# Performance work log

Measured on AMD Instinct MI355X. Metric: run time of the kernel, lower is better.

The kernel has to match this reference:

```python
import jax, jax.numpy as jnp
import numpy as np

MAX_STEPS = 20  # matches init kwarg max_steps


def gru_cell(x, h, W_ih, W_hh, b_ih, b_hh):
    # PyTorch GRUCell: gates ordered (reset, update, new)
    H = h.shape[1]
    gx = x @ W_ih.T + b_ih          # [B, 3H]
    gh = h @ W_hh.T + b_hh          # [B, 3H]
    r = jax.nn.sigmoid(gx[:, :H] + gh[:, :H])
    z = jax.nn.sigmoid(gx[:, H:2 * H] + gh[:, H:2 * H])
    n = jnp.tanh(gx[:, 2 * H:] + r * gh[:, 2 * H:])
    return (1.0 - z) * n + z * h


def setup_inputs() -> dict:
    key = jax.random.key(0)
    ks = jax.random.split(key, 10)
    B, E, H = 2048, 512, 1024
    bound = 1.0 / np.sqrt(H)  # torch default init scale
    uni = lambda k, shape: jax.random.uniform(k, shape, jnp.float32, -bound, bound)
    return {
        "x": jax.random.normal(ks[0], (B, E), jnp.float32),
        "W_ih": uni(ks[1], (3 * H, E)),
        "W_hh": uni(ks[2], (3 * H, H)),
        "b_ih": uni(ks[3], (3 * H,)),
        "b_hh": uni(ks[4], (3 * H,)),
        "w_out": uni(ks[5], (H,)),
        "b_out": uni(ks[6], (1,)),
        "w_lam": uni(ks[7], (H,)),
        "b_lam": uni(ks[8], (1,)),
        "u": jax.random.uniform(ks[9], (MAX_STEPS, B), jnp.float32),  # bernoulli draws
    }


def reference(x, W_ih, W_hh, b_ih, b_hh, w_out, b_out, w_lam, b_lam, u):
    B = x.shape[0]
    dt = x.dtype
    H = W_hh.shape[1]
    h0 = gru_cell(x, jnp.zeros((B, H), dt), W_ih, W_hh, b_ih, b_hh)
    steps = jnp.arange(1, MAX_STEPS + 1)

    def step(carry, inp):
        h, un_halted, halted, p_m, y_m = carry
        n_idx, u_n = inp
        lam_sig = jax.nn.sigmoid(h @ w_lam + b_lam[0])           # [B]
        lam = jnp.where(n_idx == MAX_STEPS, jnp.ones_like(lam_sig), lam_sig)
        y_n = h @ w_out + b_out[0]                                # [B]
        p_n = un_halted * lam
        un_halted = un_halted * (1.0 - lam)
        halt = (u_n < lam).astype(dt) * (1.0 - halted)            # bernoulli(lam)
        p_m = p_m * (1.0 - halt) + p_n * halt
        y_m = y_m * (1.0 - halt) + y_n * halt
        halted = halted + halt
        h = gru_cell(x, h, W_ih, W_hh, b_ih, b_hh)
        return (h, un_halted, halted, p_m, y_m), (p_n, y_n)

    init = (h0,
            jnp.ones((B,), dt),
            jnp.zeros((B,), dt),
            jnp.zeros((B,), dt),
            jnp.zeros((B,), dt))
    (_, _, _, p_m, y_m), (p, y) = jax.lax.scan(step, init, (steps, u))
    return p, y, p_m, y_m
```

## Files before the change

### kernel.cpp

```cpp
#include <hip/hip_runtime.h>
#include <math.h>


#define B_N 2048
#define E_N 512
#define H_N 1024
#define G3  3072
#define NSTEPS 20
#define BK 32
#define NT (H_N / BK)

typedef __attribute__((ext_vector_type(8))) _Float16 f16x8;
typedef __attribute__((ext_vector_type(4))) _Float16 f16x4v;
typedef __attribute__((ext_vector_type(4))) float    f32x4;

#define GLDS(src, dst) \
  __builtin_amdgcn_global_load_lds( \
      (const __attribute__((address_space(1))) void*)(src), \
      (__attribute__((address_space(3))) void*)(dst), 16, 0, 0)

__device__ __forceinline__ float sigmoidf_(float x) { return 1.0f / (1.0f + expf(-x)); }

__global__ __launch_bounds__(256, 1)
void gemm_step_mfma(const _Float16* __restrict__ h_hi_in,
                    const _Float16* __restrict__ h_lo_in,
                    const _Float16* __restrict__ Whi,
                    const _Float16* __restrict__ Wlo,
                    const float* __restrict__ b_hh,
                    const float* __restrict__ gx,
                    _Float16* __restrict__ h_hi_out,
                    _Float16* __restrict__ h_lo_out)
{
  __shared__ _Float16 lds[2][20480];

  const int tid  = threadIdx.x;
  const int lane = tid & 63;
  const int wv   = tid >> 6;
  const int wr   = wv >> 1;
  const int wc   = wv & 1;
  const int row0 = blockIdx.y * 128;
  const int col0 = blockIdx.x * 64;

  const _Float16* srcp[10];
  int ldsoff[10];
  #pragma unroll
  for (int j = 0; j < 10; ++j) {
    const int c   = wv * 10 + j;
    const int seg = (lane & 3) * 8;
    const _Float16* s;
    if (c < 8) {
      const int row = c * 16 + (lane >> 2);
      s = h_hi_in + (size_t)(row0 + row) * H_N + seg;
    } else if (c < 16) {
      const int row = (c - 8) * 16 + (lane >> 2);
      s = h_lo_in + (size_t)(row0 + row) * H_N + seg;
    } else if (c < 28) {
      const int br   = (c - 16) * 16 + (lane >> 2);
      const int wrow = (br >> 6) * H_N + col0 + (br & 63);
      s = Whi + (size_t)wrow * H_N + seg;
    } else {
      const int br   = (c - 28) * 16 + (lane >> 2);
      const int wrow = (br >> 6) * H_N + col0 + (br & 63);
      s = Wlo + (size_t)wrow * H_N + seg;
    }
    srcp[j]   = s;
    ldsoff[j] = c * 512;
  }

  f32x4 acc[3][4][2];
  #pragma unroll
  for (int g = 0; g < 3; ++g)
    #pragma unroll
    for (int mi = 0; mi < 4; ++mi)
      #pragma unroll
      for (int ni = 0; ni < 2; ++ni)
        acc[g][mi][ni] = (f32x4){0.f, 0.f, 0.f, 0.f};

  const int lrow = lane & 15;
  const int lk   = (lane >> 4) * 8;

  #pragma unroll
  for (int j = 0; j < 10; ++j) {
    GLDS(srcp[j], &lds[0][ldsoff[j]]);
    srcp[j] += BK;
  }
  __syncthreads();

  for (int t = 0; t < NT; ++t) {
    const int p = t & 1;
    if (t + 1 < NT) {
      #pragma unroll
      for (int j = 0; j < 10; ++j) {
        GLDS(srcp[j], &lds[p ^ 1][ldsoff[j]]);
        srcp[j] += BK;
      }
    }
    f16x8 ah[4], al[4];
    #pragma unroll
    for (int mi = 0; mi < 4; ++mi) {
      const int r = wr * 64 + mi * 16 + lrow;
      ah[mi] = *(const f16x8*)&lds[p][r * 32 + lk];
      al[mi] = *(const f16x8*)&lds[p][4096 + r * 32 + lk];
    }
    f16x8 bh[3][2], bl[3][2];
    #pragma unroll
    for (int g = 0; g < 3; ++g)
      #pragma unroll
      for (int ni = 0; ni < 2; ++ni) {
        const int r = g * 64 + wc * 32 + ni * 16 + lrow;
        bh[g][ni] = *(const f16x8*)&lds[p][8192 + r * 32 + lk];
        bl[g][ni] = *(const f16x8*)&lds[p][14336 + r * 32 + lk];
      }
    #pragma unroll
    for (int g = 0; g < 3; ++g)
      #pragma unroll
      for (int mi = 0; mi < 4; ++mi)
        #pragma unroll
        for (int ni = 0; ni < 2; ++ni) {
          f32x4 c = acc[g][mi][ni];
          c = __builtin_amdgcn_mfma_f32_16x16x32_f16(ah[mi], bh[g][ni], c, 0, 0, 0);
          c = __builtin_amdgcn_mfma_f32_16x16x32_f16(ah[mi], bl[g][ni], c, 0, 0, 0);
          c = __builtin_amdgcn_mfma_f32_16x16x32_f16(al[mi], bh[g][ni], c, 0, 0, 0);
          acc[g][mi][ni] = c;
        }
    __syncthreads();
  }

  #pragma unroll
  for (int mi = 0; mi < 4; ++mi) {
    #pragma unroll
    for (int ni = 0; ni < 2; ++ni) {
      const int n = col0 + wc * 32 + ni * 16 + lrow;
      const float bhr = b_hh[n];
      const float bhz = b_hh[H_N + n];
      const float bhn = b_hh[2 * H_N + n];
      #pragma unroll
      for (int r = 0; r < 4; ++r) {
        const int m = row0 + wr * 64 + mi * 16 + (lane >> 4) * 4 + r;
        const float gr = acc[0][mi][ni][r] + bhr;
        const float gz = acc[1][mi][ni][r] + bhz;
        const float gn = acc[2][mi][ni][r] + bhn;
        const size_t gxb = (size_t)m * G3;
        const float rr = sigmoidf_(gx[gxb + n] + gr);
        const float zz = sigmoidf_(gx[gxb + H_N + n] + gz);
        const float nn = tanhf(gx[gxb + 2 * H_N + n] + rr * gn);
        const size_t hidx = (size_t)m * H_N + n;
        const float hold = (float)h_hi_in[hidx] + (float)h_lo_in[hidx];
        const float hf = (1.f - zz) * nn + zz * hold;
        const _Float16 hh = (_Float16)hf;
        h_hi_out[hidx] = hh;
        h_lo_out[hidx] = (_Float16)(hf - (float)hh);
      }
    }
  }
}

__global__ __launch_bounds__(256)
void split_whh_kernel(const float* __restrict__ W_hh,
                      _Float16* __restrict__ Whi, _Float16* __restrict__ Wlo)
{
  const size_t base = ((size_t)blockIdx.x * 256 + threadIdx.x) * 4;
  const float4 w = *(const float4*)&W_hh[base];
  float s[4] = {w.x, w.y, w.z, w.w};
  f16x4v hi, lo;
  #pragma unroll
  for (int e = 0; e < 4; ++e) {
    const _Float16 h = (_Float16)s[e];
    hi[e] = h;
    lo[e] = (_Float16)(s[e] - (float)h);
  }
  *(f16x4v*)&Whi[base] = hi;
  *(f16x4v*)&Wlo[base] = lo;
}

__global__ __launch_bounds__(256)
void gemm_gx_kernel(const float* __restrict__ x,
                    const float* __restrict__ W_ih,
                    const float* __restrict__ b_ih,
                    float* __restrict__ gx)
{
    __shared__ float As[16][68];
    __shared__ float Bs[16][68];
    const int tid = threadIdx.x;
    const int tx = tid & 15, ty = tid >> 4;
    const int row0 = blockIdx.y * 64;
    const int col0 = blockIdx.x * 64;
    const int lr = tid >> 2;
    const int lk = (tid & 3) << 2;
    float acc[4][4] = {};
    for (int k0 = 0; k0 < E_N; k0 += 16) {
        float4 av = *(const float4*)(x    + (size_t)(row0 + lr) * E_N + k0 + lk);
        float4 bv = *(const float4*)(W_ih + (size_t)(col0 + lr) * E_N + k0 + lk);
        As[lk+0][lr] = av.x; As[lk+1][lr] = av.y; As[lk+2][lr] = av.z; As[lk+3][lr] = av.w;
        Bs[lk+0][lr] = bv.x; Bs[lk+1][lr] = bv.y; Bs[lk+2][lr] = bv.z; Bs[lk+3][lr] = bv.w;
        __syncthreads();
        #pragma unroll
        for (int k = 0; k < 16; ++k) {
            float4 a4 = *(const float4*)&As[k][ty << 2];
            float4 b4 = *(const float4*)&Bs[k][tx << 2];
            float aa[4] = {a4.x, a4.y, a4.z, a4.w};
            float bb[4] = {b4.x, b4.y, b4.z, b4.w};
            #pragma unroll
            for (int i = 0; i < 4; ++i)
                #pragma unroll
                for (int j = 0; j < 4; ++j)
                    acc[i][j] = fmaf(aa[i], bb[j], acc[i][j]);
        }
        __syncthreads();
    }
    #pragma unroll
    for (int i = 0; i < 4; ++i) {
        const int r = row0 + (ty << 2) + i;
        #pragma unroll
        for (int j = 0; j < 4; ++j) {
            const int c = col0 + (tx << 2) + j;
            gx[(size_t)r * G3 + c] = acc[i][j] + b_ih[c];
        }
    }
}

__global__ __launch_bounds__(256)
void init_h0_kernel(const float* __restrict__ gx, const float* __restrict__ b_hh,
                    _Float16* __restrict__ h_hi, _Float16* __restrict__ h_lo,
                    float* __restrict__ states)
{
    const int idx = blockIdx.x * 256 + threadIdx.x;
    const int r = idx >> 10;
    const int c = idx & (H_N - 1);
    const float rr = sigmoidf_(gx[(size_t)r * G3 + c] + b_hh[c]);
    const float zz = sigmoidf_(gx[(size_t)r * G3 + H_N + c] + b_hh[H_N + c]);
    const float nn = tanhf(gx[(size_t)r * G3 + 2 * H_N + c] + rr * b_hh[2 * H_N + c]);
    const float hf = (1.0f - zz) * nn;
    const _Float16 hh = (_Float16)hf;
    h_hi[idx] = hh;
    h_lo[idx] = (_Float16)(hf - (float)hh);
    if (idx < B_N) {
        states[idx]           = 1.0f;
        states[B_N + idx]     = 0.0f;
        states[2 * B_N + idx] = 0.0f;
        states[3 * B_N + idx] = 0.0f;
    }
}

__global__ __launch_bounds__(256)
void halt_kernel(const int n,
                 const _Float16* __restrict__ h_hi, const _Float16* __restrict__ h_lo,
                 const float* __restrict__ w_out, const float* __restrict__ b_out,
                 const float* __restrict__ w_lam, const float* __restrict__ b_lam,
                 const float* __restrict__ u,
                 float* __restrict__ states,
                 float* __restrict__ out_p, float* __restrict__ out_y,
                 float* __restrict__ out_pm, float* __restrict__ out_ym)
{
    const int row = blockIdx.x;
    const int tid = threadIdx.x;
    const size_t base = (size_t)row * H_N + (tid << 2);
    const f16x4v hh4 = *(const f16x4v*)&h_hi[base];
    const f16x4v hl4 = *(const f16x4v*)&h_lo[base];
    const float4 wl = *(const float4*)&w_lam[tid << 2];
    const float4 wo = *(const float4*)&w_out[tid << 2];
    float hv[4];
    #pragma unroll
    for (int e = 0; e < 4; ++e) hv[e] = (float)hh4[e] + (float)hl4[e];
    float s_lam = hv[0] * wl.x + hv[1] * wl.y + hv[2] * wl.z + hv[3] * wl.w;
    float s_out = hv[0] * wo.x + hv[1] * wo.y + hv[2] * wo.z + hv[3] * wo.w;
    #pragma unroll
    for (int off = 32; off > 0; off >>= 1) {
        s_lam += __shfl_down(s_lam, off);
        s_out += __shfl_down(s_out, off);
    }
    __shared__ float redl[4], redo[4];
    const int wid = tid >> 6;
    if ((tid & 63) == 0) { redl[wid] = s_lam; redo[wid] = s_out; }
    __syncthreads();
    if (tid == 0) {
        const float dlam = redl[0] + redl[1] + redl[2] + redl[3];
        const float dout = redo[0] + redo[1] + redo[2] + redo[3];
        const float lam = (n == NSTEPS) ? 1.0f : sigmoidf_(dlam + b_lam[0]);
        const float y_n = dout + b_out[0];
        float un = states[row];
        float ha = states[B_N + row];
        float pm = states[2 * B_N + row];
        float ym = states[3 * B_N + row];
        const float p_n = un * lam;
        un = un * (1.0f - lam);
        const float halt = (u[(size_t)(n - 1) * B_N + row] < lam ? 1.0f : 0.0f) * (1.0f - ha);
        pm = pm * (1.0f - halt) + p_n * halt;
        ym = ym * (1.0f - halt) + y_n * halt;
        ha += halt;
        states[row] = un;
        states[B_N + row] = ha;
        states[2 * B_N + row] = pm;
        states[3 * B_N + row] = ym;
        out_p[(size_t)(n - 1) * B_N + row] = p_n;
        out_y[(size_t)(n - 1) * B_N + row] = y_n;
        if (n == NSTEPS) { out_pm[row] = pm; out_ym[row] = ym; }
    }
}

extern "C" void kernel_launch(void* const* d_in, const int* in_sizes, int n_in,
                              void* d_out, int out_size, void* d_ws, size_t ws_size,
                              hipStream_t stream) {
    const float* x     = (const float*)d_in[0];
    const float* W_ih  = (const float*)d_in[1];
    const float* W_hh  = (const float*)d_in[2];
    const float* b_ih  = (const float*)d_in[3];
    const float* b_hh  = (const float*)d_in[4];
    const float* w_out = (const float*)d_in[5];
    const float* b_out = (const float*)d_in[6];
    const float* w_lam = (const float*)d_in[7];
    const float* b_lam = (const float*)d_in[8];
    const float* u     = (const float*)d_in[9];

    float* out_p  = (float*)d_out;
    float* out_y  = out_p + (size_t)NSTEPS * B_N;
    float* out_pm = out_y + (size_t)NSTEPS * B_N;
    float* out_ym = out_pm + B_N;

    float* ws = (float*)d_ws;
    float*     gx   = ws;
    _Float16*  Whi  = (_Float16*)(gx + (size_t)B_N * G3);
    _Float16*  Wlo  = Whi + (size_t)G3 * H_N;
    _Float16*  hAhi = Wlo + (size_t)G3 * H_N;
    _Float16*  hAlo = hAhi + (size_t)B_N * H_N;
    _Float16*  hBhi = hAlo + (size_t)B_N * H_N;
    _Float16*  hBlo = hBhi + (size_t)B_N * H_N;
    float*     states = (float*)(hBlo + (size_t)B_N * H_N);

    const dim3 blk(256);
    split_whh_kernel<<<dim3((size_t)G3 * H_N / 1024), blk, 0, stream>>>(W_hh, Whi, Wlo);
    gemm_gx_kernel<<<dim3(G3 / 64, B_N / 64), blk, 0, stream>>>(x, W_ih, b_ih, gx);
    init_h0_kernel<<<dim3(B_N * H_N / 256), blk, 0, stream>>>(gx, b_hh, hAhi, hAlo, states);

    _Float16 *hchi = hAhi, *hclo = hAlo, *hnhi = hBhi, *hnlo = hBlo;
    for (int n = 1; n <= NSTEPS; ++n) {
        halt_kernel<<<dim3(B_N), blk, 0, stream>>>(n, hchi, hclo, w_out, b_out, w_lam, b_lam, u,
                                                   states, out_p, out_y, out_pm, out_ym);
        if (n < NSTEPS) {
            gemm_step_mfma<<<dim3(H_N / 64, B_N / 128), blk, 0, stream>>>(
                hchi, hclo, Whi, Wlo, b_hh, gx, hnhi, hnlo);
            _Float16* t;
            t = hchi; hchi = hnhi; hnhi = t;
            t = hclo; hclo = hnlo; hnlo = t;
        }
    }
}
```

Before: 1.282 ms.

## Fuse halting dot products into GRU step GEMM, narrow tiles, MFMA input GEMM

Result: no change. 1.286 ms (+0.3%).

```diff
diff --git a/kernel.cpp b/kernel.cpp
--- a/kernel.cpp
+++ b/kernel.cpp
@@ -8,7 +8,9 @@
 #define G3  3072
 #define NSTEPS 20
 #define BK 32
-#define NT (H_N / BK)
+#define NT_H (H_N / BK)
+#define NT_E (E_N / BK)
+#define NCB  (H_N / 32)
 
 typedef __attribute__((ext_vector_type(8))) _Float16 f16x8;
 typedef __attribute__((ext_vector_type(4))) _Float16 f16x4v;
@@ -21,17 +23,157 @@
 
 __device__ __forceinline__ float sigmoidf_(float x) { return 1.0f / (1.0f + expf(-x)); }
 
-__global__ __launch_bounds__(256, 1)
+__global__ __launch_bounds__(256, 2)
 void gemm_step_mfma(const _Float16* __restrict__ h_hi_in,
                     const _Float16* __restrict__ h_lo_in,
                     const _Float16* __restrict__ Whi,
                     const _Float16* __restrict__ Wlo,
                     const float* __restrict__ b_hh,
                     const float* __restrict__ gx,
+                    const float* __restrict__ w_lam,
+                    const float* __restrict__ w_out,
                     _Float16* __restrict__ h_hi_out,
-                    _Float16* __restrict__ h_lo_out)
-{
-  __shared__ _Float16 lds[2][20480];
+                    _Float16* __restrict__ h_lo_out,
+                    float* __restrict__ part_lam,
+                    float* __restrict__ part_out)
+{
+  __shared__ _Float16 lds[2][14336];
+  __shared__ float pl_red[128][2], po_red[128][2];
+
+  const int tid  = threadIdx.x;
+  const int lane = tid & 63;
+  const int wv   = tid >> 6;
+  const int wr   = wv >> 1;
+  const int wc   = wv & 1;
+  const int row0 = blockIdx.y * 128;
+  const int col0 = blockIdx.x * 32;
+  const int cb   = blockIdx.x;
+
+  const _Float16* srcp[7];
+  int ldsoff[7];
+  #pragma unroll
+  for (int j = 0; j < 7; ++j) {
+    const int c     = wv * 7 + j;
+    const int seg   = (lane & 3) * 8;
+    const int row16 = lane >> 2;
+    const _Float16* s;
+    if (c < 8) {
+      s = h_hi_in + (size_t)(row0 + c * 16 + row16) * H_N + seg;
+    } else if (c < 16) {
+      s = h_lo_in + (size_t)(row0 + (c - 8) * 16 + row16) * H_N + seg;
+    } else if (c < 22) {
+      const int br = (c - 16) * 16 + row16;
+      s = Whi + (size_t)((br >> 5) * H_N + col0 + (br & 31)) * H_N + seg;
+    } else {
+      const int br = (c - 22) * 16 + row16;
+      s = Wlo + (size_t)((br >> 5) * H_N + col0 + (br & 31)) * H_N + seg;
+    }
+    srcp[j]   = s;
+    ldsoff[j] = c * 512;
+  }
+
+  f32x4 acc[3][4];
+  #pragma unroll
+  for (int g = 0; g < 3; ++g)
+    #pragma unroll
+    for (int mi = 0; mi < 4; ++mi)
+      acc[g][mi] = (f32x4){0.f, 0.f, 0.f, 0.f};
+
+  const int lrow = lane & 15;
+  const int lk   = (lane >> 4) * 8;
+  const int q    = lane >> 4;
+
+  #pragma unroll
+  for (int j = 0; j < 7; ++j) { GLDS(srcp[j], &lds[0][ldsoff[j]]); srcp[j] += BK; }
+  __syncthreads();
+
+  for (int t = 0; t < NT_H; ++t) {
+    const int p = t & 1;
+    if (t + 1 < NT_H) {
+      #pragma unroll
+      for (int j = 0; j < 7; ++j) { GLDS(srcp[j], &lds[p ^ 1][ldsoff[j]]); srcp[j] += BK; }
+    }
+    f16x8 ah[4], al[4];
+    #pragma unroll
+    for (int mi = 0; mi < 4; ++mi) {
+      const int r = wr * 64 + mi * 16 + lrow;
+      ah[mi] = *(const f16x8*)&lds[p][r * 32 + lk];
+      al[mi] = *(const f16x8*)&lds[p][4096 + r * 32 + lk];
+    }
+    f16x8 bh[3], bl[3];
+    #pragma unroll
+    for (int g = 0; g < 3; ++g) {
+      const int r = g * 32 + wc * 16 + lrow;
+      bh[g] = *(const f16x8*)&lds[p][8192 + r * 32 + lk];
+      bl[g] = *(const f16x8*)&lds[p][11264 + r * 32 + lk];
+    }
+    #pragma unroll
+    for (int g = 0; g < 3; ++g)
+      #pragma unroll
+      for (int mi = 0; mi < 4; ++mi) {
+        f32x4 c = acc[g][mi];
+        c = __builtin_amdgcn_mfma_f32_16x16x32_f16(ah[mi], bh[g], c, 0, 0, 0);
+        c = __builtin_amdgcn_mfma_f32_16x16x32_f16(ah[mi], bl[g], c, 0, 0, 0);
+        c = __builtin_amdgcn_mfma_f32_16x16x32_f16(al[mi], bh[g], c, 0, 0, 0);
+        acc[g][mi] = c;
+      }
+    __syncthreads();
+  }
+
+  const int n   = col0 + wc * 16 + lrow;
+  const float bhr = b_hh[n];
+  const float bhz = b_hh[H_N + n];
+  const float bhn = b_hh[2 * H_N + n];
+  const float wl  = w_lam[n];
+  const float wo  = w_out[n];
+  #pragma unroll
+  for (int mi = 0; mi < 4; ++mi) {
+    #pragma unroll
+    for (int r = 0; r < 4; ++r) {
+      const int m = row0 + wr * 64 + mi * 16 + q * 4 + r;
+      const float gr = acc[0][mi][r] + bhr;
+      const float gz = acc[1][mi][r] + bhz;
+      const float gn = acc[2][mi][r] + bhn;
+      const size_t gxb = (size_t)m * G3;
+      const float rr = sigmoidf_(gx[gxb + n] + gr);
+      const float zz = sigmoidf_(gx[gxb + H_N + n] + gz);
+      const float nn = tanhf(gx[gxb + 2 * H_N + n] + rr * gn);
+      const size_t hidx = (size_t)m * H_N + n;
+      const float hold = (float)h_hi_in[hidx] + (float)h_lo_in[hidx];
+      const float hf = (1.f - zz) * nn + zz * hold;
+      const _Float16 hh = (_Float16)hf;
+      h_hi_out[hidx] = hh;
+      h_lo_out[hidx] = (_Float16)(hf - (float)hh);
+      float pl = hf * wl;
+      float po = hf * wo;
+      #pragma unroll
+      for (int mk = 1; mk < 16; mk <<= 1) {
+        pl += __shfl_xor(pl, mk);
+        po += __shfl_xor(po, mk);
+      }
+      if (lrow == 0) {
+        pl_red[wr * 64 + mi * 16 + q * 4 + r][wc] = pl;
+        po_red[wr * 64 + mi * 16 + q * 4 + r][wc] = po;
+      }
+    }
+  }
+  __syncthreads();
+  if (tid < 128) {
+    const int m = row0 + tid;
+    part_lam[(size_t)cb * B_N + m] = pl_red[tid][0] + pl_red[tid][1];
+    part_out[(size_t)cb * B_N + m] = po_red[tid][0] + po_red[tid][1];
+  }
+}
+
+__global__ __launch_bounds__(256, 3)
+void gemm_gx_mfma(const _Float16* __restrict__ xhi,
+                  const _Float16* __restrict__ xlo,
+                  const _Float16* __restrict__ Wihhi,
+                  const _Float16* __restrict__ Wihlo,
+                  const float* __restrict__ b_ih,
+                  float* __restrict__ gx)
+{
+  __shared__ _Float16 lds[2][12288];
 
   const int tid  = threadIdx.x;
   const int lane = tid & 63;
@@ -41,59 +183,41 @@
   const int row0 = blockIdx.y * 128;
   const int col0 = blockIdx.x * 64;
 
-  const _Float16* srcp[10];
-  int ldsoff[10];
-  #pragma unroll
-  for (int j = 0; j < 10; ++j) {
-    const int c   = wv * 10 + j;
-    const int seg = (lane & 3) * 8;
+  const _Float16* srcp[6];
+  int ldsoff[6];
+  #pragma unroll
+  for (int j = 0; j < 6; ++j) {
+    const int c     = wv * 6 + j;
+    const int seg   = (lane & 3) * 8;
+    const int row16 = lane >> 2;
     const _Float16* s;
-    if (c < 8) {
-      const int row = c * 16 + (lane >> 2);
-      s = h_hi_in + (size_t)(row0 + row) * H_N + seg;
-    } else if (c < 16) {
-      const int row = (c - 8) * 16 + (lane >> 2);
-      s = h_lo_in + (size_t)(row0 + row) * H_N + seg;
-    } else if (c < 28) {
-      const int br   = (c - 16) * 16 + (lane >> 2);
-      const int wrow = (br >> 6) * H_N + col0 + (br & 63);
-      s = Whi + (size_t)wrow * H_N + seg;
-    } else {
-      const int br   = (c - 28) * 16 + (lane >> 2);
-      const int wrow = (br >> 6) * H_N + col0 + (br & 63);
-      s = Wlo + (size_t)wrow * H_N + seg;
-    }
+    if (c < 8)       s = xhi   + (size_t)(row0 + c * 16 + row16) * E_N + seg;
+    else if (c < 16) s = xlo   + (size_t)(row0 + (c - 8) * 16 + row16) * E_N + seg;
+    else if (c < 20) s = Wihhi + (size_t)(col0 + (c - 16) * 16 + row16) * E_N + seg;
+    else             s = Wihlo + (size_t)(col0 + (c - 20) * 16 + row16) * E_N + seg;
     srcp[j]   = s;
     ldsoff[j] = c * 512;
   }
 
-  f32x4 acc[3][4][2];
-  #pragma unroll
-  for (int g = 0; g < 3; ++g)
-    #pragma unroll
-    for (int mi = 0; mi < 4; ++mi)
-      #pragma unroll
-      for (int ni = 0; ni < 2; ++ni)
-        acc[g][mi][ni] = (f32x4){0.f, 0.f, 0.f, 0.f};
+  f32x4 acc[4][2];
+  #pragma unroll
+  for (int mi = 0; mi < 4; ++mi)
+    #pragma unroll
+    for (int ni = 0; ni < 2; ++ni) acc[mi][ni] = (f32x4){0.f, 0.f, 0.f, 0.f};
 
   const int lrow = lane & 15;
   const int lk   = (lane >> 4) * 8;
-
-  #pragma unroll
-  for (int j = 0; j < 10; ++j) {
-    GLDS(srcp[j], &lds[0][ldsoff[j]]);
-    srcp[j] += BK;
-  }
+  const int q    = lane >> 4;
+
+  #pragma unroll
+  for (int j = 0; j < 6; ++j) { GLDS(srcp[j], &lds[0][ldsoff[j]]); srcp[j] += BK; }
   __syncthreads();
 
-  for (int t = 0; t < NT; ++t) {
+  for (int t = 0; t < NT_E; ++t) {
     const int p = t & 1;
-    if (t + 1 < NT) {
-      #pragma unroll
-      for (int j = 0; j < 10; ++j) {
-        GLDS(srcp[j], &lds[p ^ 1][ldsoff[j]]);
-        srcp[j] += BK;
-      }
+    if (t + 1 < NT_E) {
+      #pragma unroll
+      for (int j = 0; j < 6; ++j) { GLDS(srcp[j], &lds[p ^ 1][ldsoff[j]]); srcp[j] += BK; }
     }
     f16x8 ah[4], al[4];
     #pragma unroll
@@ -102,27 +226,23 @@
       ah[mi] = *(const f16x8*)&lds[p][r * 32 + lk];
       al[mi] = *(const f16x8*)&lds[p][4096 + r * 32 + lk];
     }
-    f16x8 bh[3][2], bl[3][2];
-    #pragma unroll
-    for (int g = 0; g < 3; ++g)
+    f16x8 bh[2], bl[2];
+    #pragma unroll
+    for (int ni = 0; ni < 2; ++ni) {
+      const int r = wc * 32 + ni * 16 + lrow;
+      bh[ni] = *(const f16x8*)&lds[p][8192 + r * 32 + lk];
+      bl[ni] = *(const f16x8*)&lds[p][10240 + r * 32 + lk];
+    }
+    #pragma unroll
+    for (int mi = 0; mi < 4; ++mi)
       #pragma unroll
       for (int ni = 0; ni < 2; ++ni) {
-        const int r = g * 64 + wc * 32 + ni * 16 + lrow;
-        bh[g][ni] = *(const f16x8*)&lds[p][8192 + r * 32 + lk];
-        bl[g][ni] = *(const f16x8*)&lds[p][14336 + r * 32 + lk];
+        f32x4 c = acc[mi][ni];
+        c = __builtin_amdgcn_mfma_f32_16x16x32_f16(ah[mi], bh[ni], c, 0, 0, 0);
+        c = __builtin_amdgcn_mfma_f32_16x16x32_f16(ah[mi], bl[ni], c, 0, 0, 0);
+        c = __builtin_amdgcn_mfma_f32_16x16x32_f16(al[mi], bh[ni], c, 0, 0, 0);
+        acc[mi][ni] = c;
       }
-    #pragma unroll
-    for (int g = 0; g < 3; ++g)
-      #pragma unroll
-      for (int mi = 0; mi < 4; ++mi)
-        #pragma unroll
-        for (int ni = 0; ni < 2; ++ni) {
-          f32x4 c = acc[g][mi][ni];
-          c = __builtin_amdgcn_mfma_f32_16x16x32_f16(ah[mi], bh[g][ni], c, 0, 0, 0);
-          c = __builtin_amdgcn_mfma_f32_16x16x32_f16(ah[mi], bl[g][ni], c, 0, 0, 0);
-          c = __builtin_amdgcn_mfma_f32_16x16x32_f16(al[mi], bh[g][ni], c, 0, 0, 0);
-          acc[g][mi][ni] = c;
-        }
     __syncthreads();
   }
 
@@ -131,92 +251,32 @@
     #pragma unroll
     for (int ni = 0; ni < 2; ++ni) {
       const int n = col0 + wc * 32 + ni * 16 + lrow;
-      const float bhr = b_hh[n];
-      const float bhz = b_hh[H_N + n];
-      const float bhn = b_hh[2 * H_N + n];
+      const float bi = b_ih[n];
       #pragma unroll
       for (int r = 0; r < 4; ++r) {
-        const int m = row0 + wr * 64 + mi * 16 + (lane >> 4) * 4 + r;
-        const float gr = acc[0][mi][ni][r] + bhr;
-        const float gz = acc[1][mi][ni][r] + bhz;
-        const float gn = acc[2][mi][ni][r] + bhn;
-        const size_t gxb = (size_t)m * G3;
-        const float rr = sigmoidf_(gx[gxb + n] + gr);
-        const float zz = sigmoidf_(gx[gxb + H_N + n] + gz);
-        const float nn = tanhf(gx[gxb + 2 * H_N + n] + rr * gn);
-        const size_t hidx = (size_t)m * H_N + n;
-        const float hold = (float)h_hi_in[hidx] + (float)h_lo_in[hidx];
-        const float hf = (1.f - zz) * nn + zz * hold;
-        const _Float16 hh = (_Float16)hf;
-        h_hi_out[hidx] = hh;
-        h_lo_out[hidx] = (_Float16)(hf - (float)hh);
+        const int m = row0 + wr * 64 + mi * 16 + q * 4 + r;
+        gx[(size_t)m * G3 + n] = acc[mi][ni][r] + bi;
       }
     }
   }
 }
 
 __global__ __launch_bounds__(256)
-void split_whh_kernel(const float* __restrict__ W_hh,
-                      _Float16* __restrict__ Whi, _Float16* __restrict__ Wlo)
+void split_f32_kernel(const float* __restrict__ src,
+                      _Float16* __restrict__ hi, _Float16* __restrict__ lo)
 {
   const size_t base = ((size_t)blockIdx.x * 256 + threadIdx.x) * 4;
-  const float4 w = *(const float4*)&W_hh[base];
+  const float4 w = *(const float4*)&src[base];
   float s[4] = {w.x, w.y, w.z, w.w};
-  f16x4v hi, lo;
+  f16x4v h4, l4;
   #pragma unroll
   for (int e = 0; e < 4; ++e) {
     const _Float16 h = (_Float16)s[e];
-    hi[e] = h;
-    lo[e] = (_Float16)(s[e] - (float)h);
-  }
-  *(f16x4v*)&Whi[base] = hi;
-  *(f16x4v*)&Wlo[base] = lo;
-}
-
-__global__ __launch_bounds__(256)
-void gemm_gx_kernel(const float* __restrict__ x,
-                    const float* __restrict__ W_ih,
-                    const float* __restrict__ b_ih,
-                    float* __restrict__ gx)
-{
-    __shared__ float As[16][68];
-    __shared__ float Bs[16][68];
-    const int tid = threadIdx.x;
-    const int tx = tid & 15, ty = tid >> 4;
-    const int row0 = blockIdx.y * 64;
-    const int col0 = blockIdx.x * 64;
-    const int lr = tid >> 2;
-    const int lk = (tid & 3) << 2;
-    float acc[4][4] = {};
-    for (int k0 = 0; k0 < E_N; k0 += 16) {
-        float4 av = *(const float4*)(x    + (size_t)(row0 + lr) * E_N + k0 + lk);
-        float4 bv = *(const float4*)(W_ih + (size_t)(col0 + lr) * E_N + k0 + lk);
-        As[lk+0][lr] = av.x; As[lk+1][lr] = av.y; As[lk+2][lr] = av.z; As[lk+3][lr] = av.w;
-        Bs[lk+0][lr] = bv.x; Bs[lk+1][lr] = bv.y; Bs[lk+2][lr] = bv.z; Bs[lk+3][lr] = bv.w;
-        __syncthreads();
-        #pragma unroll
-        for (int k = 0; k < 16; ++k) {
-            float4 a4 = *(const float4*)&As[k][ty << 2];
-            float4 b4 = *(const float4*)&Bs[k][tx << 2];
-            float aa[4] = {a4.x, a4.y, a4.z, a4.w};
-            float bb[4] = {b4.x, b4.y, b4.z, b4.w};
-            #pragma unroll
-            for (int i = 0; i < 4; ++i)
-                #pragma unroll
-                for (int j = 0; j < 4; ++j)
-                    acc[i][j] = fmaf(aa[i], bb[j], acc[i][j]);
-        }
-        __syncthreads();
-    }
-    #pragma unroll
-    for (int i = 0; i < 4; ++i) {
-        const int r = row0 + (ty << 2) + i;
-        #pragma unroll
-        for (int j = 0; j < 4; ++j) {
-            const int c = col0 + (tx << 2) + j;
-            gx[(size_t)r * G3 + c] = acc[i][j] + b_ih[c];
-        }
-    }
+    h4[e] = h;
+    l4[e] = (_Float16)(s[e] - (float)h);
+  }
+  *(f16x4v*)&hi[base] = h4;
+  *(f16x4v*)&lo[base] = l4;
 }
 
 __global__ __launch_bounds__(256)
@@ -298,6 +358,44 @@
     }
 }
 
+__global__ __launch_bounds__(256)
+void finish_halt_kernel(const int n,
+                        const float* __restrict__ part_lam,
+                        const float* __restrict__ part_out,
+                        const float* __restrict__ b_out, const float* __restrict__ b_lam,
+                        const float* __restrict__ u,
+                        float* __restrict__ states,
+                        float* __restrict__ out_p, float* __restrict__ out_y,
+                        float* __restrict__ out_pm, float* __restrict__ out_ym)
+{
+    const int row = blockIdx.x * 256 + threadIdx.x;
+    float dlam = 0.f, dout = 0.f;
+    #pragma unroll
+    for (int cb = 0; cb < NCB; ++cb) {
+        dlam += part_lam[(size_t)cb * B_N + row];
+        dout += part_out[(size_t)cb * B_N + row];
+    }
+    const float lam = (n == NSTEPS) ? 1.0f : sigmoidf_(dlam + b_lam[0]);
+    const float y_n = dout + b_out[0];
+    float un = states[row];
+    float ha = states[B_N + row];
+    float pm = states[2 * B_N + row];
+    float ym = states[3 * B_N + row];
+    const float p_n = un * lam;
+    un = un * (1.0f - lam);
+    const float halt = (u[(size_t)(n - 1) * B_N + row] < lam ? 1.0f : 0.0f) * (1.0f - ha);
+    pm = pm * (1.0f - halt) + p_n * halt;
+    ym = ym * (1.0f - halt) + y_n * halt;
+    ha += halt;
+    states[row] = un;
+    states[B_N + row] = ha;
+    states[2 * B_N + row] = pm;
+    states[3 * B_N + row] = ym;
+    out_p[(size_t)(n - 1) * B_N + row] = p_n;
+    out_y[(size_t)(n - 1) * B_N + row] = y_n;
+    if (n == NSTEPS) { out_pm[row] = pm; out_ym[row] = ym; }
+}
+
 extern "C" void kernel_launch(void* const* d_in, const int* in_sizes, int n_in,
                               void* d_out, int out_size, void* d_ws, size_t ws_size,
                               hipStream_t stream) {
@@ -325,20 +423,31 @@
     _Float16*  hAlo = hAhi + (size_t)B_N * H_N;
     _Float16*  hBhi = hAlo + (size_t)B_N * H_N;
     _Float16*  hBlo = hBhi + (size_t)B_N * H_N;
-    float*     states = (float*)(hBlo + (size_t)B_N * H_N);
+    float*     part_lam = (float*)(hBlo + (size_t)B_N * H_N);
+    float*     part_out = part_lam + (size_t)NCB * B_N;
+    float*     states   = part_out + (size_t)NCB * B_N;
 
     const dim3 blk(256);
-    split_whh_kernel<<<dim3((size_t)G3 * H_N / 1024), blk, 0, stream>>>(W_hh, Whi, Wlo);
-    gemm_gx_kernel<<<dim3(G3 / 64, B_N / 64), blk, 0, stream>>>(x, W_ih, b_ih, gx);
+    split_f32_kernel<<<dim3((size_t)G3 * H_N / 1024), blk, 0, stream>>>(W_hh, Whi, Wlo);
+    split_f32_kernel<<<dim3((size_t)G3 * E_N / 1024), blk, 0, stream>>>(W_ih, hAhi, hAlo);
+    split_f32_kernel<<<dim3((size_t)B_N * E_N / 1024), blk, 0, stream>>>(x, hBhi, hBlo);
+    gemm_gx_mfma<<<dim3(G3 / 64, B_N / 128), blk, 0, stream>>>(hBhi, hBlo, hAhi, hAlo, b_ih, gx);
     init_h0_kernel<<<dim3(B_N * H_N / 256), blk, 0, stream>>>(gx, b_hh, hAhi, hAlo, states);
 
     _Float16 *hchi = hAhi, *hclo = hAlo, *hnhi = hBhi, *hnlo = hBlo;
     for (int n = 1; n <= NSTEPS; ++n) {
-        halt_kernel<<<dim3(B_N), blk, 0, stream>>>(n, hchi, hclo, w_out, b_out, w_lam, b_lam, u,
-                                                   states, out_p, out_y, out_pm, out_ym);
+        if (n == 1) {
+            halt_kernel<<<dim3(B_N), blk, 0, stream>>>(n, hchi, hclo, w_out, b_out,
+                                                       w_lam, b_lam, u, states,
+                                                       out_p, out_y, out_pm, out_ym);
+        } else {
+            finish_halt_kernel<<<dim3(B_N / 256), blk, 0, stream>>>(n, part_lam, part_out,
+                                                                    b_out, b_lam, u, states,
+                                                                    out_p, out_y, out_pm, out_ym);
+        }
         if (n < NSTEPS) {
-            gemm_step_mfma<<<dim3(H_N / 64, B_N / 128), blk, 0, stream>>>(
-                hchi, hclo, Whi, Wlo, b_hh, gx, hnhi, hnlo);
+            gemm_step_mfma<<<dim3(H_N / 32, B_N / 128), blk, 0, stream>>>(
+                hchi, hclo, Whi, Wlo, b_hh, gx, w_lam, w_out, hnhi, hnlo, part_lam, part_out);
             _Float16* t;
             t = hchi; hchi = hnhi; hnhi = t;
             t = hclo; hclo = hnlo; hnlo = t;
```
